# Performance work log

Hardware: AMD Instinct MI355X
Metric: run time of the kernel (lower is better)

The kernel has to match this reference:

```python
import jax, jax.numpy as jnp
import numpy as np

N = 16384
K = 16

def _w(k, shape):
    return jax.random.normal(k, shape, jnp.float32) * 0.05

def setup_inputs() -> dict:
    key = jax.random.key(0)
    ks = jax.random.split(key, 20)
    return {
        "img_feat": jax.random.normal(ks[0], (1, 32, N), jnp.float32),
        "cloud": jax.random.uniform(ks[1], (1, N, 3), jnp.float32),
        "conv1_w": _w(ks[2], (64, 32)),   "conv1_b": _w(ks[3], (64,)),
        "conv2_w": _w(ks[4], (128, 64)),  "conv2_b": _w(ks[5], (128,)),
        "psconv1_w": _w(ks[6], (256, 128)), "psconv1_b": _w(ks[7], (256,)),
        "psconv2_w": _w(ks[8], (128, 256)), "psconv2_b": _w(ks[9], (128,)),
        "pconv1_w": _w(ks[10], (64, 3)),  "pconv1_b": _w(ks[11], (64,)),
        "pconv2_w": _w(ks[12], (128, 64)),"pconv2_b": _w(ks[13], (128,)),
        "final_w": _w(ks[14], (32, 416)), "final_b": _w(ks[15], (32,)),
        "topk": K,
    }

def reference(img_feat, cloud, conv1_w, conv1_b, conv2_w, conv2_b,
              psconv1_w, psconv1_b, psconv2_w, psconv2_b,
              pconv1_w, pconv1_b, pconv2_w, pconv2_b,
              final_w, final_b, topk):
    lrelu = lambda x: jax.nn.leaky_relu(x, 0.01)
    pts = cloud[0]            # [N,3]  (module assumes bs=1)
    imf = img_feat[0].T       # [N,32]
    # point MLP: pconv1 -> lrelu -> pconv2 (Conv1d kernel=1 == per-point linear)
    cf = lrelu(pts @ pconv1_w.T + pconv1_b) @ pconv2_w.T + pconv2_b  # [N,128]
    # KNN: k smallest euclidean distances (self included)
    sq = jnp.sum(pts * pts, axis=-1)                 # [N]
    d2 = sq[:, None] + sq[None, :] - 2.0 * (pts @ pts.T)  # [N,N]
    _, idx = jax.lax.top_k(-d2, topk)                # [N,K]
    nb_pts = pts[idx]                                # [N,K,3]
    dist = jnp.sqrt(jnp.maximum(jnp.sum((pts[:, None, :] - nb_pts) ** 2, -1), 1e-12))
    wgt = jax.nn.softmax(-dist, axis=1)              # [N,K]
    nb_img = imf[idx]                                # [N,K,32]
    nb_cf = cf[idx]                                  # [N,K,128]
    sf = lrelu(nb_img @ conv1_w.T + conv1_b) @ conv2_w.T + conv2_b         # [N,K,128]
    sfp = lrelu(nb_cf @ psconv1_w.T + psconv1_b) @ psconv2_w.T + psconv2_b # [N,K,128]
    sf = jnp.max(sf * wgt[:, :, None], axis=1)       # weighted max-pool -> [N,128]
    sfp = jnp.max(sfp * wgt[:, :, None], axis=1)     # [N,128]
    final = jnp.concatenate([sfp, imf, sf, cf], axis=1)  # [N,416]
    out = lrelu(final) @ final_w.T + final_b         # [N,32]
    return out.T[None]                               # [1,32,N]
```

## Files before the change

### kernel.cpp

```cpp
#include <hip/hip_runtime.h>
#include <math.h>

#define N 16384
#define KNN 16
#define G 14
#define NCELL (G * G * G)

typedef __attribute__((ext_vector_type(8))) short bf16x8;
typedef __attribute__((ext_vector_type(4))) float f32x4;
typedef unsigned short ushort_t;
typedef unsigned long long u64;

__device__ __forceinline__ float lrelu(float a) { return a > 0.f ? a : 0.01f * a; }

__device__ __forceinline__ ushort_t f2bf(float f) {
  unsigned u = __float_as_uint(f);
  u += 0x7FFF + ((u >> 16) & 1);
  return (ushort_t)(u >> 16);
}
__device__ __forceinline__ float bf2f(ushort_t h) {
  return __uint_as_float((unsigned)h << 16);
}
__device__ __forceinline__ float bflo(unsigned u) {
  return __uint_as_float(u << 16);
}
__device__ __forceinline__ float bfhi(unsigned u) {
  return __uint_as_float(u & 0xffff0000u);
}
__device__ __forceinline__ int lanerank(u64 mask) {
  return __builtin_amdgcn_mbcnt_hi((unsigned)(mask >> 32),
         __builtin_amdgcn_mbcnt_lo((unsigned)mask, 0));
}
__device__ __forceinline__ int cellof(float x) {
  int c = (int)(x * (float)G);
  return c < 0 ? 0 : (c > G - 1 ? G - 1 : c);
}
__device__ __forceinline__ int cellid(float x, float y, float z) {
  return (cellof(z) * G + cellof(y)) * G + cellof(x);
}

#define PPB 64
__global__ __launch_bounds__(256) void prepw_kernel(
    const float* __restrict__ img, const float* __restrict__ cloud,
    const float* __restrict__ p1w, const float* __restrict__ p1b,
    const float* __restrict__ p2w, const float* __restrict__ p2b,
    const float* __restrict__ ps1w, const float* __restrict__ ps2w,
    const float* __restrict__ c1w, const float* __restrict__ c2w,
    const float* __restrict__ fw,
    float4* __restrict__ pts4, ushort_t* __restrict__ cfh,
    ushort_t* __restrict__ imfh,
    ushort_t* __restrict__ w1h, ushort_t* __restrict__ w2h,
    ushort_t* __restrict__ c1h, ushort_t* __restrict__ c2h,
    float* __restrict__ fwp2, int* __restrict__ count) {
  int t = threadIdx.x;
  if (blockIdx.x >= 256) {
    int e = (blockIdx.x - 256) * 256 + t;
    if (e < 32768) w1h[e] = f2bf(ps1w[e]);
    else if (e < 65536) w2h[e - 32768] = f2bf(ps2w[e - 32768]);
    else if (e < 67584) c1h[e - 65536] = f2bf(c1w[e - 65536]);
    else if (e < 75776) c2h[e - 67584] = f2bf(c2w[e - 67584]);
    else if (e < 89088) {
      int e2 = e - 75776;
      int j4 = e2 >> 7, r2 = e2 & 127;
      int ch = r2 >> 2, sub = r2 & 3;
      fwp2[e2] = fw[ch * 416 + j4 * 4 + sub];
    }
    return;
  }
  __shared__ alignas(16) float w2t[64 * 132];
  __shared__ alignas(16) float hs[PPB * 68];
  __shared__ alignas(16) float w1s[192];
  __shared__ alignas(16) float b1s[64];
  __shared__ alignas(16) float b2s[128];
  __shared__ float ptmp[PPB * 3];
  __shared__ float psx[PPB], psy[PPB], psz[PPB];
  int pb = blockIdx.x * PPB;

  for (int e = t; e < 128 * 64; e += 256) {
    int ch = e >> 6, k = e & 63;
    w2t[k * 132 + ch] = p2w[e];
  }
  if (t < 192) w1s[t] = p1w[t];
  if (t < 64) b1s[t] = p1b[t];
  if (t < 128) b2s[t] = p2b[t];
  if (t < PPB * 3) ptmp[t] = cloud[pb * 3 + t];
  __syncthreads();
  if (t < PPB) {
    float x = ptmp[t * 3], y = ptmp[t * 3 + 1], z = ptmp[t * 3 + 2];
    psx[t] = x; psy[t] = y; psz[t] = z;
    pts4[pb + t] = make_float4(x, y, z, x * x + y * y + z * z);
    atomicAdd(&count[cellid(x, y, z)], 1);
  }
  for (int e = t; e < 32 * PPB; e += 256) {
    int c = e >> 6, p = e & 63;
    imfh[(size_t)(pb + p) * 32 + c] = f2bf(img[(size_t)c * N + pb + p]);
  }
  __syncthreads();
  for (int e = t; e < PPB * 64; e += 256) {
    int pt_ = e >> 6, ch = e & 63;
    float a = b1s[ch] + psx[pt_] * w1s[ch * 3] + psy[pt_] * w1s[ch * 3 + 1] +
              psz[pt_] * w1s[ch * 3 + 2];
    hs[pt_ * 68 + ch] = lrelu(a);
  }
  __syncthreads();
  for (int e = t; e < PPB * 32; e += 256) {
    int pt_ = e >> 5, c4 = (e & 31) << 2;
    float4 acc = *(const float4*)&b2s[c4];
    const float* hrow = &hs[pt_ * 68];
    #pragma unroll
    for (int k = 0; k < 64; k += 4) {
      float4 h4 = *(const float4*)&hrow[k];
      float4 w0 = *(const float4*)&w2t[(k + 0) * 132 + c4];
      float4 w1_ = *(const float4*)&w2t[(k + 1) * 132 + c4];
      float4 w2_ = *(const float4*)&w2t[(k + 2) * 132 + c4];
      float4 w3 = *(const float4*)&w2t[(k + 3) * 132 + c4];
      acc.x = fmaf(h4.x, w0.x, fmaf(h4.y, w1_.x, fmaf(h4.z, w2_.x, fmaf(h4.w, w3.x, acc.x))));
      acc.y = fmaf(h4.x, w0.y, fmaf(h4.y, w1_.y, fmaf(h4.z, w2_.y, fmaf(h4.w, w3.y, acc.y))));
      acc.z = fmaf(h4.x, w0.z, fmaf(h4.y, w1_.z, fmaf(h4.z, w2_.z, fmaf(h4.w, w3.z, acc.z))));
      acc.w = fmaf(h4.x, w0.w, fmaf(h4.y, w1_.w, fmaf(h4.z, w2_.w, fmaf(h4.w, w3.w, acc.w))));
    }
    unsigned lo = (unsigned)f2bf(acc.x) | ((unsigned)f2bf(acc.y) << 16);
    unsigned hi = (unsigned)f2bf(acc.z) | ((unsigned)f2bf(acc.w) << 16);
    *(uint2*)&cfh[(size_t)(pb + pt_) * 128 + c4] = make_uint2(lo, hi);
  }
}

__global__ __launch_bounds__(256) void scan_kernel(
    const int* __restrict__ count, int* __restrict__ cellStart,
    int* __restrict__ cellofs) {
  __shared__ int part[256];
  int t = threadIdx.x;
  int local[11];
  int s = 0;
  #pragma unroll
  for (int j = 0; j < 11; ++j) {
    int idx = t * 11 + j;
    local[j] = s;
    s += (idx < NCELL) ? count[idx] : 0;
  }
  part[t] = s;
  __syncthreads();
  for (int off = 1; off < 256; off <<= 1) {
    int v = (t >= off) ? part[t - off] : 0;
    __syncthreads();
    part[t] += v;
    __syncthreads();
  }
  int base = part[t] - s;
  #pragma unroll
  for (int j = 0; j < 11; ++j) {
    int idx = t * 11 + j;
    int v = base + local[j];
    if (idx < NCELL) { cellStart[idx] = v; cellofs[idx] = v; }
  }
  if (t == 255) cellStart[NCELL] = part[255];
}

__global__ __launch_bounds__(256) void scatter_kernel(
    const float4* __restrict__ pts4, int* __restrict__ cellofs,
    float4* __restrict__ spts) {
  int p = blockIdx.x * 256 + threadIdx.x;
  float4 v = pts4[p];
  int pos = atomicAdd(&cellofs[cellid(v.x, v.y, v.z)], 1);
  spts[pos] = make_float4(v.x, v.y, v.z, __int_as_float(p));
}

#define NB_LD 136
#define S1_LD 264
#define NI_LD 40
#define H1_LD 72
__global__ __launch_bounds__(256) void ymlp_kernel(
    const ushort_t* __restrict__ cfh, const ushort_t* __restrict__ imfh,
    const ushort_t* __restrict__ w1h, const float* __restrict__ b1,
    const ushort_t* __restrict__ w2h, const float* __restrict__ b2,
    const ushort_t* __restrict__ c1h, const float* __restrict__ c1b,
    const ushort_t* __restrict__ c2h, const float* __restrict__ c2b,
    ushort_t* __restrict__ ycf, ushort_t* __restrict__ yimg) {
  __shared__ ushort_t nb[64 * NB_LD];
  __shared__ ushort_t s1[64 * S1_LD];
  int t = threadIdx.x;
  int w = t >> 6, lane = t & 63;
  int col = lane & 15, quad = lane >> 4;

  if (blockIdx.x < 256) {
    int pbase = blockIdx.x * 64;
    for (int e = t; e < 1024; e += 256) {
      int row = e >> 4, c8 = (e & 15) << 3;
      *(uint4*)&nb[row * NB_LD + c8] =
          *(const uint4*)&cfh[(size_t)(pbase + row) * 128 + c8];
    }
    __syncthreads();
    f32x4 acc1[4][4];
    #pragma unroll
    for (int tt = 0; tt < 4; ++tt)
      #pragma unroll
      for (int p = 0; p < 4; ++p) acc1[tt][p] = (f32x4){0.f, 0.f, 0.f, 0.f};
    for (int k0 = 0; k0 < 128; k0 += 32) {
      bf16x8 a[4];
      #pragma unroll
      for (int p = 0; p < 4; ++p)
        a[p] = *(const bf16x8*)&nb[(p * 16 + col) * NB_LD + k0 + quad * 8];
      #pragma unroll
      for (int tt = 0; tt < 4; ++tt) {
        int n = w * 64 + tt * 16 + col;
        bf16x8 b = *(const bf16x8*)&w1h[n * 128 + k0 + quad * 8];
        #pragma unroll
        for (int p = 0; p < 4; ++p)
          acc1[tt][p] = __builtin_amdgcn_mfma_f32_16x16x32_bf16(a[p], b, acc1[tt][p], 0, 0, 0);
      }
    }
    #pragma unroll
    for (int tt = 0; tt < 4; ++tt) {
      int n = w * 64 + tt * 16 + col;
      float bb = b1[n];
      #pragma unroll
      for (int p = 0; p < 4; ++p)
        #pragma unroll
        for (int r = 0; r < 4; ++r)
          s1[(p * 16 + quad * 4 + r) * S1_LD + n] = f2bf(lrelu(acc1[tt][p][r] + bb));
    }
    __syncthreads();
    f32x4 acc2[2][4];
    #pragma unroll
    for (int tt = 0; tt < 2; ++tt)
      #pragma unroll
      for (int p = 0; p < 4; ++p) acc2[tt][p] = (f32x4){0.f, 0.f, 0.f, 0.f};
    for (int k0 = 0; k0 < 256; k0 += 32) {
      bf16x8 a[4];
      #pragma unroll
      for (int p = 0; p < 4; ++p)
        a[p] = *(const bf16x8*)&s1[(p * 16 + col) * S1_LD + k0 + quad * 8];
      #pragma unroll
      for (int tt = 0; tt < 2; ++tt) {
        int n = w * 32 + tt * 16 + col;
        bf16x8 b = *(const bf16x8*)&w2h[n * 256 + k0 + quad * 8];
        #pragma unroll
        for (int p = 0; p < 4; ++p)
          acc2[tt][p] = __builtin_amdgcn_mfma_f32_16x16x32_bf16(a[p], b, acc2[tt][p], 0, 0, 0);
      }
    }
    #pragma unroll
    for (int tt = 0; tt < 2; ++tt) {
      int n = w * 32 + tt * 16 + col;
      float bb = b2[n];
      #pragma unroll
      for (int p = 0; p < 4; ++p)
        #pragma unroll
        for (int r = 0; r < 4; ++r)
          ycf[(size_t)(pbase + p * 16 + quad * 4 + r) * 128 + n] =
              f2bf(acc2[tt][p][r] + bb);
    }
  } else {
    int pbase = (blockIdx.x - 256) * 64;
    ushort_t* nbi = nb;
    ushort_t* h1 = s1;
    {
      int row = t >> 2, c8 = (t & 3) << 3;
      *(uint4*)&nbi[row * NI_LD + c8] =
          *(const uint4*)&imfh[(size_t)(pbase + row) * 32 + c8];
    }
    __syncthreads();
    {
      f32x4 accA[4];
      #pragma unroll
      for (int p = 0; p < 4; ++p) accA[p] = (f32x4){0.f, 0.f, 0.f, 0.f};
      int n = w * 16 + col;
      bf16x8 b = *(const bf16x8*)&c1h[n * 32 + quad * 8];
      #pragma unroll
      for (int p = 0; p < 4; ++p) {
        bf16x8 a = *(const bf16x8*)&nbi[(p * 16 + col) * NI_LD + quad * 8];
        accA[p] = __builtin_amdgcn_mfma_f32_16x16x32_bf16(a, b, accA[p], 0, 0, 0);
      }
      __syncthreads();
      float bb = c1b[n];
      #pragma unroll
      for (int p = 0; p < 4; ++p)
        #pragma unroll
        for (int r = 0; r < 4; ++r)
          h1[(p * 16 + quad * 4 + r) * H1_LD + n] = f2bf(lrelu(accA[p][r] + bb));
    }
    __syncthreads();
    f32x4 acc2[2][4];
    #pragma unroll
    for (int tt = 0; tt < 2; ++tt)
      #pragma unroll
      for (int p = 0; p < 4; ++p) acc2[tt][p] = (f32x4){0.f, 0.f, 0.f, 0.f};
    for (int k0 = 0; k0 < 64; k0 += 32) {
      bf16x8 a[4];
      #pragma unroll
      for (int p = 0; p < 4; ++p)
        a[p] = *(const bf16x8*)&h1[(p * 16 + col) * H1_LD + k0 + quad * 8];
      #pragma unroll
      for (int tt = 0; tt < 2; ++tt) {
        int n = w * 32 + tt * 16 + col;
        bf16x8 b = *(const bf16x8*)&c2h[n * 64 + k0 + quad * 8];
        #pragma unroll
        for (int p = 0; p < 4; ++p)
          acc2[tt][p] = __builtin_amdgcn_mfma_f32_16x16x32_bf16(a[p], b, acc2[tt][p], 0, 0, 0);
      }
    }
    #pragma unroll
    for (int tt = 0; tt < 2; ++tt) {
      int n = w * 32 + tt * 16 + col;
      float bb = c2b[n];
      #pragma unroll
      for (int p = 0; p < 4; ++p)
        #pragma unroll
        for (int r = 0; r < 4; ++r)
          yimg[(size_t)(pbase + p * 16 + quad * 4 + r) * 128 + n] =
              f2bf(acc2[tt][p][r] + bb);
    }
  }
}

__device__ __forceinline__ float tadj(float tau, float qw) {
  float a = tau - qw;
  return a + fabsf(a) * 2e-7f + 1e-35f;
}

template <int NS>
__device__ __forceinline__ u64 selimpl(u64* buf, int cnt, int lane,
                                       float& tau) {
  u64 v[NS];
  unsigned k[NS];
  #pragma unroll
  for (int s = 0; s < NS; ++s) {
    int idx = s * 64 + lane;
    v[s] = (idx < cnt) ? buf[idx] : ~0ULL;
    k[s] = (unsigned)(v[s] >> 32);
  }
  unsigned m = 0u;
  #pragma unroll
  for (int b = 31; b >= 0; --b) {
    unsigned probe = m | (1u << b);
    int c = 0;
    #pragma unroll
    for (int s = 0; s < NS; ++s) c += __popcll(__ballot(k[s] < probe));
    if (c < KNN) m = probe;
  }
  int c_lt = 0, ne = 0;
  bool e[NS];
  #pragma unroll
  for (int s = 0; s < NS; ++s) {
    c_lt += __popcll(__ballot(k[s] < m));
    e[s] = (k[s] == m);
    ne += __popcll(__ballot(e[s]));
  }
  int need_eq = KNN - c_lt;
  unsigned m2 = 0xFFFFFFFFu;
  if (ne != need_eq) {
    m2 = 0u;
    #pragma unroll
    for (int b = 13; b >= 0; --b) {
      unsigned probe = m2 | (1u << b);
      int c = 0;
      #pragma unroll
      for (int s = 0; s < NS; ++s)
        c += __popcll(__ballot(e[s] && ((unsigned)v[s] < probe)));
      if (c < need_eq) m2 = probe;
    }
  }
  int base = 0;
  #pragma unroll
  for (int s = 0; s < NS; ++s) {
    bool sel = (k[s] < m) || (e[s] && ((unsigned)v[s] <= m2));
    u64 msk = __ballot(sel);
    if (sel) buf[base + lanerank(msk)] = v[s];
    base += __popcll(msk);
  }
  tau = __uint_as_float(m);
  if (!(tau == tau)) tau = INFINITY;
  return buf[lane & 15];
}

__device__ __forceinline__ u64 select16(u64* buf, int& cnt, int lane,
                                        float& tau) {
  u64 r = (cnt <= 64) ? selimpl<1>(buf, cnt, lane, tau)
                      : selimpl<2>(buf, cnt, lane, tau);
  cnt = KNN;
  return r;
}

__global__ __launch_bounds__(256) void knng_kernel(
    const float4* __restrict__ pts4, const float4* __restrict__ spts,
    const int* __restrict__ cellStart,
    const ushort_t* __restrict__ ycf, const ushort_t* __restrict__ yimg,
    const ushort_t* __restrict__ cfh, const ushort_t* __restrict__ imfh,
    const float* __restrict__ fwp2, const float* __restrict__ fb,
    float* __restrict__ outT) {
  __shared__ u64 sbuf[4][128];
  __shared__ alignas(16) float feat[4][416];
  int t = threadIdx.x;
  int wv = t >> 6, lane = t & 63;
  int sblk = (blockIdx.x & 7) * 512 + (blockIdx.x >> 3);
  int sid = sblk * 4 + wv;
  u64* buf = sbuf[wv];

  float4 q = spts[sid];
  int pid = __float_as_int(q.w);
  float qw = fmaf(q.z, q.z, fmaf(q.y, q.y, q.x * q.x));
  float q2x = -2.f * q.x, q2y = -2.f * q.y, q2z = -2.f * q.z;
  int cx = cellof(q.x), cy = cellof(q.y), cz = cellof(q.z);

  float tau;
  {
    const float r0 = 0.0758f;
    float rr = r0;
    #pragma unroll
    for (int it = 0; it < 2; ++it) {
      float fx = (fminf(q.x + rr, 1.f) - fmaxf(q.x - rr, 0.f)) * (0.5f / rr);
      float fy = (fminf(q.y + rr, 1.f) - fmaxf(q.y - rr, 0.f)) * (0.5f / rr);
      float fz = (fminf(q.z + rr, 1.f) - fmaxf(q.z - rr, 0.f)) * (0.5f / rr);
      rr = r0 * __powf(fx * fy * fz, -0.333333f);
    }
    rr *= 1.05f;
    tau = rr * rr;
  }
  u64 vres;

  for (int r = 1;; ++r) {
    int lx = max(cx - r, 0), hx = min(cx + r, G - 1);
    int ly = max(cy - r, 0), hy = min(cy + r, G - 1);
    int lz = max(cz - r, 0), hz = min(cz + r, G - 1);
    int ny = hy - ly + 1, nz = hz - lz + 1, nruns = ny * nz;
    int cnt = 0;
    float ta = tadj(tau, qw);

    for (int rb = 0; rb < nruns; rb += 64) {
      int ln = rb + lane;
      int rs = 0, rc = 0;
      if (ln < nruns) {
        int z = lz + ln / ny, y = ly + ln % ny;
        int row = (z * G + y) * G;
        rs = cellStart[row + lx];
        rc = cellStart[row + hx + 1] - rs;
      }
      int nr = nruns - rb; nr = nr > 64 ? 64 : nr;
      int off = rc;
      #pragma unroll
      for (int d = 1; d < 64; d <<= 1) {
        int v = __shfl_up(off, d);
        if (lane >= d) off += v;
      }
      int T = __shfl(off, 63);
      off -= rc;

      for (int cb = 0; cb < T; cb += 64) {
        int rk = cb + lane;
        int j = 0;
        if (nr <= 16) {
          #pragma unroll
          for (int step = 8; step; step >>= 1) {
            int nj = j + step;
            if (__shfl(off, nj) <= rk) j = nj;
          }
        } else if (nr <= 32) {
          #pragma unroll
          for (int step = 16; step; step >>= 1) {
            int nj = j + step;
            if (__shfl(off, nj) <= rk) j = nj;
          }
        } else {
          #pragma unroll
          for (int step = 32; step; step >>= 1) {
            int nj = j + step;
            if (__shfl(off, nj) <= rk) j = nj;
          }
        }
        int src = __shfl(rs, j) + rk - __shfl(off, j);
        bool valid = rk < T;
        if (!valid) src = 0;
        float4 c = spts[src];
        float cw = fmaf(c.z, c.z, fmaf(c.y, c.y, c.x * c.x));
        float d2 = fmaf(q2x, c.x, fmaf(q2y, c.y, fmaf(q2z, c.z, cw)));
        bool pass = valid && (d2 <= ta);
        u64 mask = __ballot(pass);
        if (mask) {
          if (pass) {
            int oid = __float_as_int(c.w);
            u64 key = ((u64)__float_as_uint(fmaxf(d2 + qw, 0.f)) << 32) | (unsigned)oid;
            buf[cnt + lanerank(mask)] = key;
          }
          cnt += __popcll(mask);
          if (cnt > 64) {
            select16(buf, cnt, lane, tau);
            ta = tadj(tau, qw);
          }
        }
      }
    }
    u64 v = select16(buf, cnt, lane, tau);
    float cl = INFINITY;
    if (lx > 0)     cl = fminf(cl, q.x - (float)lx / (float)G);
    if (hx < G - 1) cl = fminf(cl, (float)(hx + 1) / (float)G - q.x);
    if (ly > 0)     cl = fminf(cl, q.y - (float)ly / (float)G);
    if (hy < G - 1) cl = fminf(cl, (float)(hy + 1) / (float)G - q.y);
    if (lz > 0)     cl = fminf(cl, q.z - (float)lz / (float)G);
    if (hz < G - 1) cl = fminf(cl, (float)(hz + 1) / (float)G - q.z);
    bool full = (lx == 0 && hx == G - 1 && ly == 0 && hy == G - 1 &&
                 lz == 0 && hz == G - 1);
    if (full || tau * 1.00002f <= cl * cl) { vres = v; break; }
  }

  int myid = (lane < KNN) ? (int)(unsigned)(vres & 0xffffffffULL) : 0;
  float mywg = 0.f;
  {
    float4 c = pts4[myid];
    float dx = q.x - c.x, dy = q.y - c.y, dz = q.z - c.z;
    float dist = sqrtf(fmaxf(dx * dx + dy * dy + dz * dz, 1e-12f));
    float md = (lane < KNN) ? dist : INFINITY;
    #pragma unroll
    for (int off = 1; off < KNN; off <<= 1) md = fminf(md, __shfl_xor(md, off));
    float e = __expf(md - dist);
    float se = (lane < KNN) ? e : 0.f;
    #pragma unroll
    for (int off = 1; off < KNN; off <<= 1) se += __shfl_xor(se, off);
    mywg = e / se;
  }

  int ksub = lane >> 4, c8 = lane & 15;
  float vimf = (lane < 32) ? bf2f(imfh[(size_t)pid * 32 + lane]) : 0.f;
  unsigned vcf = *(const unsigned*)&cfh[(size_t)pid * 128 + lane * 2];

  float a0[8], a1[8];
  #pragma unroll
  for (int j = 0; j < 8; ++j) { a0[j] = -INFINITY; a1[j] = -INFINITY; }
  #pragma unroll
  for (int kk = 0; kk < 4; ++kk) {
    int k = kk * 4 + ksub;
    int id = __shfl(myid, k);
    float wg = __shfl(mywg, k);
    uint4 v = *(const uint4*)&ycf[(size_t)id * 128 + c8 * 8];
    uint4 u = *(const uint4*)&yimg[(size_t)id * 128 + c8 * 8];
    unsigned vv[4] = {v.x, v.y, v.z, v.w};
    unsigned uu[4] = {u.x, u.y, u.z, u.w};
    #pragma unroll
    for (int h = 0; h < 4; ++h) {
      a0[h * 2]     = fmaxf(a0[h * 2],     bflo(vv[h]) * wg);
      a0[h * 2 + 1] = fmaxf(a0[h * 2 + 1], bfhi(vv[h]) * wg);
      a1[h * 2]     = fmaxf(a1[h * 2],     bflo(uu[h]) * wg);
      a1[h * 2 + 1] = fmaxf(a1[h * 2 + 1], bfhi(uu[h]) * wg);
    }
  }
  #pragma unroll
  for (int j = 0; j < 8; ++j) {
    a0[j] = fmaxf(a0[j], __shfl_xor(a0[j], 16));
    a0[j] = fmaxf(a0[j], __shfl_xor(a0[j], 32));
    a1[j] = fmaxf(a1[j], __shfl_xor(a1[j], 16));
    a1[j] = fmaxf(a1[j], __shfl_xor(a1[j], 32));
  }
  if (lane < 16) {
    #pragma unroll
    for (int j = 0; j < 8; ++j) {
      feat[wv][c8 * 8 + j] = lrelu(a0[j]);
      feat[wv][160 + c8 * 8 + j] = lrelu(a1[j]);
    }
  }
  if (lane < 32) feat[wv][128 + lane] = lrelu(vimf);
  feat[wv][288 + lane * 2] = lrelu(bflo(vcf));
  feat[wv][288 + lane * 2 + 1] = lrelu(bfhi(vcf));

  int ch = lane & 31, half = lane >> 5;
  float acc = half ? 0.f : fb[ch];
  const float* wr = fwp2 + (half * 52) * 128 + ch * 4;
  const float* fr = &feat[wv][half * 208];
  #pragma unroll 4
  for (int j4 = 0; j4 < 52; ++j4) {
    float4 w4 = *(const float4*)(wr + j4 * 128);
    float4 f4 = *(const float4*)(fr + j4 * 4);
    acc = fmaf(f4.x, w4.x, fmaf(f4.y, w4.y, fmaf(f4.z, w4.z, fmaf(f4.w, w4.w, acc))));
  }
  acc += __shfl_xor(acc, 32);
  if (lane < 32) outT[(size_t)pid * 32 + ch] = acc;
}

__global__ __launch_bounds__(256) void tran_kernel(
    const float* __restrict__ outT, float* __restrict__ out) {
  __shared__ float tile[32][129];
  int t = threadIdx.x;
  int pbase = blockIdx.x * 128;
  #pragma unroll
  for (int i = 0; i < 16; ++i) {
    int e = i * 256 + t;
    int p = e >> 5, c = e & 31;
    tile[c][p] = outT[(size_t)(pbase + p) * 32 + c];
  }
  __syncthreads();
  #pragma unroll
  for (int i = 0; i < 16; ++i) {
    int e = i * 256 + t;
    int c = e >> 7, p = e & 127;
    out[(size_t)c * N + pbase + p] = tile[c][p];
  }
}

extern "C" void kernel_launch(void* const* d_in, const int* in_sizes, int n_in,
                              void* d_out, int out_size, void* d_ws, size_t ws_size,
                              hipStream_t stream) {
  const float* img   = (const float*)d_in[0];
  const float* cloud = (const float*)d_in[1];
  const float* c1w   = (const float*)d_in[2];
  const float* c1b   = (const float*)d_in[3];
  const float* c2w   = (const float*)d_in[4];
  const float* c2b   = (const float*)d_in[5];
  const float* ps1w  = (const float*)d_in[6];
  const float* ps1b  = (const float*)d_in[7];
  const float* ps2w  = (const float*)d_in[8];
  const float* ps2b  = (const float*)d_in[9];
  const float* p1w   = (const float*)d_in[10];
  const float* p1b   = (const float*)d_in[11];
  const float* p2w   = (const float*)d_in[12];
  const float* p2b   = (const float*)d_in[13];
  const float* fw    = (const float*)d_in[14];
  const float* fb    = (const float*)d_in[15];
  float* out = (float*)d_out;

  char* ws = (char*)d_ws;
  float4*   pts4  = (float4*)(ws + 0);
  ushort_t* cfh   = (ushort_t*)(ws + 262144);
  ushort_t* imfh  = (ushort_t*)(ws + 4456448);
  ushort_t* w1h   = (ushort_t*)(ws + 7602176);
  ushort_t* w2h   = (ushort_t*)(ws + 7667712);
  ushort_t* c1h   = (ushort_t*)(ws + 7733248);
  ushort_t* c2h   = (ushort_t*)(ws + 7737344);
  ushort_t* ycf   = (ushort_t*)(ws + 7753472);
  ushort_t* yimg  = (ushort_t*)(ws + 11947776);
  float4*   spts  = (float4*)(ws + 16142080);
  int*      cellStart = (int*)(ws + 16404224);
  int*      cellofs   = (int*)(ws + 16436992);
  int*      count     = (int*)(ws + 16453376);
  float*    fwp2      = (float*)(ws + 16469760);
  float*    outT      = (float*)(ws + 16523008);

  hipMemsetAsync(count, 0, NCELL * sizeof(int), stream);
  prepw_kernel<<<604, 256, 0, stream>>>(img, cloud, p1w, p1b, p2w, p2b,
                                        ps1w, ps2w, c1w, c2w, fw,
                                        pts4, cfh, imfh, w1h, w2h, c1h, c2h,
                                        fwp2, count);
  scan_kernel<<<1, 256, 0, stream>>>(count, cellStart, cellofs);
  scatter_kernel<<<64, 256, 0, stream>>>(pts4, cellofs, spts);
  ymlp_kernel<<<512, 256, 0, stream>>>(cfh, imfh, w1h, ps1b, w2h, ps2b,
                                       c1h, c1b, c2h, c2b, ycf, yimg);
  knng_kernel<<<N / 4, 256, 0, stream>>>(pts4, spts, cellStart,
                                         ycf, yimg, cfh, imfh,
                                         fwp2, fb, outT);
  tran_kernel<<<N / 128, 256, 0, stream>>>(outT, out);
}
```

Baseline: 179.2 us.

## Move final linear layer to bf16 MFMA kernel writing transposed output

The final 416->32 linear layer is taken out of the KNN kernel. The KNN kernel now writes the pooled 416-wide feature row per point as bf16 to a workspace buffer. A new kernel runs that GEMM with 16x16x32 bf16 MFMA and writes the channel-major output directly, which replaces both the per-wave scalar FMA loop and the separate transpose kernel. The neighbor distance for the softmax weights is also reused from the high bits of the selection key instead of reloading the neighbor coordinates. In exchange, the change adds a feature round-trip through global memory and bf16 rounding of the final features and weights.

```diff
diff --git a/kernel.cpp b/kernel.cpp
--- a/kernel.cpp
+++ b/kernel.cpp
@@ -51,7 +51,7 @@
     ushort_t* __restrict__ imfh,
     ushort_t* __restrict__ w1h, ushort_t* __restrict__ w2h,
     ushort_t* __restrict__ c1h, ushort_t* __restrict__ c2h,
-    float* __restrict__ fwp2, int* __restrict__ count) {
+    ushort_t* __restrict__ fwh, int* __restrict__ count) {
   int t = threadIdx.x;
   if (blockIdx.x >= 256) {
     int e = (blockIdx.x - 256) * 256 + t;
@@ -61,9 +61,7 @@
     else if (e < 75776) c2h[e - 67584] = f2bf(c2w[e - 67584]);
     else if (e < 89088) {
       int e2 = e - 75776;
-      int j4 = e2 >> 7, r2 = e2 & 127;
-      int ch = r2 >> 2, sub = r2 & 3;
-      fwp2[e2] = fw[ch * 416 + j4 * 4 + sub];
+      if (e2 < 13312) fwh[e2] = f2bf(fw[e2]);
     }
     return;
   }
@@ -382,12 +380,10 @@
 }
 
 __global__ __launch_bounds__(256) void knng_kernel(
-    const float4* __restrict__ pts4, const float4* __restrict__ spts,
-    const int* __restrict__ cellStart,
+    const float4* __restrict__ spts, const int* __restrict__ cellStart,
     const ushort_t* __restrict__ ycf, const ushort_t* __restrict__ yimg,
     const ushort_t* __restrict__ cfh, const ushort_t* __restrict__ imfh,
-    const float* __restrict__ fwp2, const float* __restrict__ fb,
-    float* __restrict__ outT) {
+    ushort_t* __restrict__ featb) {
   __shared__ u64 sbuf[4][128];
   __shared__ alignas(16) float feat[4][416];
   int t = threadIdx.x;
@@ -505,9 +501,8 @@
   int myid = (lane < KNN) ? (int)(unsigned)(vres & 0xffffffffULL) : 0;
   float mywg = 0.f;
   {
-    float4 c = pts4[myid];
-    float dx = q.x - c.x, dy = q.y - c.y, dz = q.z - c.z;
-    float dist = sqrtf(fmaxf(dx * dx + dy * dy + dz * dz, 1e-12f));
+    float dd = __uint_as_float((unsigned)(vres >> 32));
+    float dist = sqrtf(fmaxf(dd, 1e-12f));
     float md = (lane < KNN) ? dist : INFINITY;
     #pragma unroll
     for (int off = 1; off < KNN; off <<= 1) md = fminf(md, __shfl_xor(md, off));
@@ -560,37 +555,42 @@
   feat[wv][288 + lane * 2] = lrelu(bflo(vcf));
   feat[wv][288 + lane * 2 + 1] = lrelu(bfhi(vcf));
 
-  int ch = lane & 31, half = lane >> 5;
-  float acc = half ? 0.f : fb[ch];
-  const float* wr = fwp2 + (half * 52) * 128 + ch * 4;
-  const float* fr = &feat[wv][half * 208];
-  #pragma unroll 4
-  for (int j4 = 0; j4 < 52; ++j4) {
-    float4 w4 = *(const float4*)(wr + j4 * 128);
-    float4 f4 = *(const float4*)(fr + j4 * 4);
-    acc = fmaf(f4.x, w4.x, fmaf(f4.y, w4.y, fmaf(f4.z, w4.z, fmaf(f4.w, w4.w, acc))));
-  }
-  acc += __shfl_xor(acc, 32);
-  if (lane < 32) outT[(size_t)pid * 32 + ch] = acc;
-}
-
-__global__ __launch_bounds__(256) void tran_kernel(
-    const float* __restrict__ outT, float* __restrict__ out) {
-  __shared__ float tile[32][129];
+  unsigned* frow = (unsigned*)(featb + (size_t)pid * 416);
+  #pragma unroll
+  for (int it = 0; it < 4; ++it) {
+    int pi = it * 64 + lane;
+    if (pi < 208) {
+      float lo = feat[wv][pi * 2], hi = feat[wv][pi * 2 + 1];
+      frow[pi] = (unsigned)f2bf(lo) | ((unsigned)f2bf(hi) << 16);
+    }
+  }
+}
+
+__global__ __launch_bounds__(256) void fing_kernel(
+    const ushort_t* __restrict__ featb, const ushort_t* __restrict__ fwh,
+    const float* __restrict__ fb, float* __restrict__ out) {
   int t = threadIdx.x;
-  int pbase = blockIdx.x * 128;
-  #pragma unroll
-  for (int i = 0; i < 16; ++i) {
-    int e = i * 256 + t;
-    int p = e >> 5, c = e & 31;
-    tile[c][p] = outT[(size_t)(pbase + p) * 32 + c];
-  }
-  __syncthreads();
-  #pragma unroll
-  for (int i = 0; i < 16; ++i) {
-    int e = i * 256 + t;
-    int c = e >> 7, p = e & 127;
-    out[(size_t)c * N + pbase + p] = tile[c][p];
+  int wv = t >> 6, lane = t & 63;
+  int col = lane & 15, quad = lane >> 4;
+  int pbase = blockIdx.x * 64 + wv * 16;
+  f32x4 acc[2];
+  acc[0] = (f32x4){0.f, 0.f, 0.f, 0.f};
+  acc[1] = (f32x4){0.f, 0.f, 0.f, 0.f};
+  for (int k0 = 0; k0 < 416; k0 += 32) {
+    bf16x8 b = *(const bf16x8*)&featb[(size_t)(pbase + col) * 416 + k0 + quad * 8];
+    #pragma unroll
+    for (int tt = 0; tt < 2; ++tt) {
+      bf16x8 a = *(const bf16x8*)&fwh[(tt * 16 + col) * 416 + k0 + quad * 8];
+      acc[tt] = __builtin_amdgcn_mfma_f32_16x16x32_bf16(a, b, acc[tt], 0, 0, 0);
+    }
+  }
+  #pragma unroll
+  for (int tt = 0; tt < 2; ++tt) {
+    #pragma unroll
+    for (int r = 0; r < 4; ++r) {
+      int ch = tt * 16 + quad * 4 + r;
+      out[(size_t)ch * N + pbase + col] = acc[tt][r] + fb[ch];
+    }
   }
 }
 
@@ -619,30 +619,29 @@
   float4*   pts4  = (float4*)(ws + 0);
   ushort_t* cfh   = (ushort_t*)(ws + 262144);
   ushort_t* imfh  = (ushort_t*)(ws + 4456448);
-  ushort_t* w1h   = (ushort_t*)(ws + 7602176);
-  ushort_t* w2h   = (ushort_t*)(ws + 7667712);
-  ushort_t* c1h   = (ushort_t*)(ws + 7733248);
-  ushort_t* c2h   = (ushort_t*)(ws + 7737344);
-  ushort_t* ycf   = (ushort_t*)(ws + 7753472);
-  ushort_t* yimg  = (ushort_t*)(ws + 11947776);
-  float4*   spts  = (float4*)(ws + 16142080);
-  int*      cellStart = (int*)(ws + 16404224);
-  int*      cellofs   = (int*)(ws + 16436992);
-  int*      count     = (int*)(ws + 16453376);
-  float*    fwp2      = (float*)(ws + 16469760);
-  float*    outT      = (float*)(ws + 16523008);
+  ushort_t* w1h   = (ushort_t*)(ws + 5505024);
+  ushort_t* w2h   = (ushort_t*)(ws + 5570560);
+  ushort_t* c1h   = (ushort_t*)(ws + 5636096);
+  ushort_t* c2h   = (ushort_t*)(ws + 5640192);
+  ushort_t* ycf   = (ushort_t*)(ws + 5656576);
+  ushort_t* yimg  = (ushort_t*)(ws + 9850880);
+  float4*   spts  = (float4*)(ws + 14045184);
+  int*      cellStart = (int*)(ws + 14307328);
+  int*      cellofs   = (int*)(ws + 14323712);
+  int*      count     = (int*)(ws + 14339840);
+  ushort_t* fwh       = (ushort_t*)(ws + 14356224);
+  ushort_t* featb     = (ushort_t*)(ws + 14388992);
 
   hipMemsetAsync(count, 0, NCELL * sizeof(int), stream);
   prepw_kernel<<<604, 256, 0, stream>>>(img, cloud, p1w, p1b, p2w, p2b,
                                         ps1w, ps2w, c1w, c2w, fw,
                                         pts4, cfh, imfh, w1h, w2h, c1h, c2h,
-                                        fwp2, count);
+                                        fwh, count);
   scan_kernel<<<1, 256, 0, stream>>>(count, cellStart, cellofs);
   scatter_kernel<<<64, 256, 0, stream>>>(pts4, cellofs, spts);
   ymlp_kernel<<<512, 256, 0, stream>>>(cfh, imfh, w1h, ps1b, w2h, ps2b,
                                        c1h, c1b, c2h, c2b, ycf, yimg);
-  knng_kernel<<<N / 4, 256, 0, stream>>>(pts4, spts, cellStart,
-                                         ycf, yimg, cfh, imfh,
-                                         fwp2, fb, outT);
-  tran_kernel<<<N / 128, 256, 0, stream>>>(outT, out);
-}
+  knng_kernel<<<N / 4, 256, 0, stream>>>(spts, cellStart,
+                                         ycf, yimg, cfh, imfh, featb);
+  fing_kernel<<<N / 64, 256, 0, stream>>>(featb, fwh, fb, out);
+}
```

Result: faster. 171.4 us (-4.3%).
